# Kernel optimization log

Measured on AMD Instinct MI355X. Metric: run time of the kernel, lower is better.

## Reference

```python
import jax, jax.numpy as jnp
import numpy as np

T, N, E = 4, 20000, 320000
F_IN, EH, NH, GH, OUT = 12, 32, 64, 64, 1
NUM_LAYERS = 2
EB_IN = (EH + 2 * NH) * 2 + GH  # 384
NB_IN = 2 * NH + 2 * EH + GH    # 256
GB_IN = NH + EH + GH            # 160


def setup_inputs() -> dict:
    key = jax.random.key(0)
    ks = jax.random.split(key, 24)
    f32 = jnp.float32
    def w(k, fan_in, shape):
        return jax.random.normal(k, shape, f32) * (1.0 / np.sqrt(fan_in))
    return {
        "node_attr": jax.random.normal(ks[0], (T, N, F_IN), f32),
        "edge_attr": jax.random.normal(ks[1], (T, E, 1), f32),
        "edge_index": jax.random.randint(ks[2], (2, E), 0, N, jnp.int32),
        "sp_L_vals": jax.random.normal(ks[3], (E,), f32),
        "global_attr": jax.random.normal(ks[4], (1, GH), f32),
        "coeff": jnp.full((1,), 0.1, f32),
        "W_ee": w(ks[5], 1, (1, EH)), "b_ee": jnp.zeros((EH,), f32),
        "W_ne": w(ks[6], F_IN, (F_IN, NH)), "b_ne": jnp.zeros((NH,), f32),
        "W_eb": w(ks[7], EB_IN, (EB_IN, EH)), "b_eb": jnp.zeros((EH,), f32),
        "W_nb": w(ks[8], NB_IN, (NB_IN, NH)), "b_nb": jnp.zeros((NH,), f32),
        "W_gb": w(ks[9], GB_IN, (GB_IN, GH)), "b_gb": jnp.zeros((GH,), f32),
        "W_nd1": w(ks[10], NH, (NH, NH)), "b_nd1": jnp.zeros((NH,), f32),
        "W_nd2": w(ks[11], NH, (NH, OUT)), "b_nd2": jnp.zeros((OUT,), f32),
    }


def _forward(node_attr, edge_attr, edge_index, sp_L_vals, global_attr, coeff,
             W_ee, b_ee, W_ne, b_ne, W_eb, b_eb, W_nb, b_nb, W_gb, b_gb,
             W_nd1, b_nd1, W_nd2, b_nd2):
    relu = jax.nn.relu
    s, r = edge_index[0], edge_index[1]
    seg = lambda v, idx: jax.ops.segment_sum(v, idx, num_segments=N)
    c = coeff[0]

    # encoders
    x_enc = relu(node_attr @ W_ne + b_ne)   # [T,N,NH]
    e_enc = relu(edge_attr @ W_ee + b_ee)   # [T,E,EH]

    def run_gn(xT, eT, g0):
        # recurrent GN core over processing steps; hidden (h_x,h_e,h_g) starts at zeros
        def step(carry, inp):
            h_x, h_e, h_g = carry
            x_in, e_in = inp
            gE = jnp.broadcast_to(h_g, (E, GH))
            # EdgeBlock: [edge_in, edge_h, sender_in, sender_h, recv_in, recv_h, global]
            edge_cat = jnp.concatenate(
                [e_in, h_e, x_in[s], h_x[s], x_in[r], h_x[r], gE], axis=-1)
            e_new = relu(edge_cat @ W_eb + b_eb)              # [E,EH]
            sent = seg(e_new, s)                              # scatter_add by sender
            recv = seg(e_new, r)                              # scatter_add by receiver
            gN = jnp.broadcast_to(h_g, (N, GH))
            node_cat = jnp.concatenate([x_in, h_x, sent, recv, gN], axis=-1)
            x_new = relu(node_cat @ W_nb + b_nb)              # [N,NH]
            # GlobalBlock: scatter_mean == plain mean (single graph)
            g_cat = jnp.concatenate(
                [x_new.mean(0, keepdims=True), e_new.mean(0, keepdims=True), h_g], axis=-1)
            g_new = relu(g_cat @ W_gb + b_gb)                 # [1,GH]
            # physics terms (pde='diff'): time derivative = state update,
            # spatial derivative = coeff * (graph-Laplacian action via sp_L edge weights)
            t_der = x_new - h_x
            s_der = c * seg(sp_L_vals[:, None] * (x_new[s] - x_new[r]), r)
            return (x_new, e_new, g_new), (x_new, e_new, g_new, t_der, s_der)
        carry0 = (jnp.zeros((N, NH), jnp.float32), jnp.zeros((E, EH), jnp.float32), g0)
        _, ys = jax.lax.scan(step, carry0, (xT, eT))
        return ys  # xs[T,N,NH], es[T,E,EH], gs[T,1,GH], td[T,N,NH], sd[T,N,NH]

    xs, es, gs, td, sd = run_gn(x_enc, e_enc, global_attr)
    x_pre = x_enc
    for _ in range(NUM_LAYERS - 1):
        x_res = xs + x_pre          # residual node state feeds next GN layer
        x_pre = x_res
        xs, es, gs, td, sd = run_gn(x_res, es, gs[0])

    x_final = xs + x_pre            # add_residual=True final residual
    h = relu(x_final @ W_nd1 + b_nd1)
    out_nodes = h @ W_nd2 + b_nd2   # [T,N,OUT]
    return out_nodes, td, sd


def reference(node_attr, edge_attr, edge_index, sp_L_vals, global_attr, coeff,
              W_ee, b_ee, W_ne, b_ne, W_eb, b_eb, W_nb, b_nb, W_gb, b_gb,
              W_nd1, b_nd1, W_nd2, b_nd2):
    return _forward(node_attr, edge_attr, edge_index, sp_L_vals, global_attr, coeff,
                    W_ee, b_ee, W_ne, b_ne, W_eb, b_eb, W_nb, b_nb, W_gb, b_gb,
                    W_nd1, b_nd1, W_nd2, b_nd2)
```

## Files before the change

kernel.cpp:

```cpp
#include <hip/hip_runtime.h>


typedef __attribute__((ext_vector_type(8))) short s16x8;
typedef __attribute__((ext_vector_type(4))) float f32x4;

#define T_STEPS 4
#define NN 20000
#define NP 20224
#define NE 320000

__device__ __forceinline__ float bf2f(unsigned short h){
  return __uint_as_float(((unsigned)h)<<16);
}
__device__ __forceinline__ unsigned short f2bf(float f){
  unsigned u = __float_as_uint(f);
  return (unsigned short)((u + 0x7fffu + ((u>>16)&1u)) >> 16);
}
__device__ __forceinline__ float loadIn(const void* p, size_t i, int bf){
  return bf ? bf2f(((const unsigned short*)p)[i]) : ((const float*)p)[i];
}
__device__ __forceinline__ void storeOut(void* o, size_t i, float v, int bf){
  if(bf) ((unsigned short*)o)[i] = f2bf(v);
  else   ((float*)o)[i] = v;
}
__device__ __forceinline__ void load8(const float* __restrict__ p, float* v){
  const float4* q4 = (const float4*)p;
  float4 a = q4[0], b = q4[1];
  v[0]=a.x; v[1]=a.y; v[2]=a.z; v[3]=a.w;
  v[4]=b.x; v[5]=b.y; v[6]=b.z; v[7]=b.w;
}
__device__ __forceinline__ int4 pack8(const float* v){
  unsigned p0 = (unsigned)f2bf(v[0]) | ((unsigned)f2bf(v[1])<<16);
  unsigned p1 = (unsigned)f2bf(v[2]) | ((unsigned)f2bf(v[3])<<16);
  unsigned p2 = (unsigned)f2bf(v[4]) | ((unsigned)f2bf(v[5])<<16);
  unsigned p3 = (unsigned)f2bf(v[6]) | ((unsigned)f2bf(v[7])<<16);
  return make_int4((int)p0,(int)p1,(int)p2,(int)p3);
}
__device__ __forceinline__ void unp8(int4 w, float* a){
  unsigned x;
  x=(unsigned)w.x; a[0]=__uint_as_float(x<<16); a[1]=__uint_as_float(x&0xffff0000u);
  x=(unsigned)w.y; a[2]=__uint_as_float(x<<16); a[3]=__uint_as_float(x&0xffff0000u);
  x=(unsigned)w.z; a[4]=__uint_as_float(x<<16); a[5]=__uint_as_float(x&0xffff0000u);
  x=(unsigned)w.w; a[6]=__uint_as_float(x<<16); a[7]=__uint_as_float(x&0xffff0000u);
}

union I4S8 { int4 i; s16x8 s; };

__global__ void probe_kernel(const void* coeff_in, int* flagp, float* coeff_f){
  unsigned short u = ((const unsigned short*)coeff_in)[0];
  float as_bf = bf2f(u);
  int f = (fabsf(as_bf - 0.1f) < 0.02f) ? 1 : 0;
  *flagp = f;
  *coeff_f = f ? as_bf : ((const float*)coeff_in)[0];
}

struct ConvJob { const void* src; float* dst; int n; };
struct ConvJobs { ConvJob j[16]; int cnt; };

__global__ void conv_kernel(ConvJobs jobs, const int* flagp, float* z, int zn){
  int bf = *flagp;
  int tid = blockIdx.x*blockDim.x + threadIdx.x;
  int stride = gridDim.x*blockDim.x;
  for(int q=0;q<jobs.cnt;q++){
    const void* s = jobs.j[q].src; float* d = jobs.j[q].dst; int n = jobs.j[q].n;
    for(int i=tid;i<n;i+=stride) d[i] = loadIn(s, i, bf);
  }
  for(int i=tid;i<zn;i+=stride) z[i]=0.f;
}

__global__ void csr_hist(const int* __restrict__ ei, int* deg_s, int* deg_r,
                         unsigned short* __restrict__ rank_s,
                         unsigned short* __restrict__ rank_r){
  int e = blockIdx.x*256+threadIdx.x;
  rank_s[e] = (unsigned short)atomicAdd(&deg_s[ei[e]],1);
  rank_r[e] = (unsigned short)atomicAdd(&deg_r[ei[NE+e]],1);
}

__global__ void csr_scan(const int* __restrict__ deg_s, int* __restrict__ off_s,
                         const int* __restrict__ deg_r, int* __restrict__ off_r){
  const int CH = NP/256;
  const int* deg = blockIdx.x ? deg_r : deg_s;
  int* off = blockIdx.x ? off_r : off_s;
  int t = threadIdx.x;
  int base = t*CH;
  int s = 0;
  #pragma unroll 8
  for(int i=0;i<CH;i++) s += deg[base+i];
  int lane = t & 63, w = t >> 6;
  int x = s;
  #pragma unroll
  for(int o=1;o<64;o<<=1){
    int y = __shfl_up(x, o, 64);
    if(lane >= o) x += y;
  }
  __shared__ int wtot[4];
  if(lane==63) wtot[w] = x;
  __syncthreads();
  int wbase = 0;
  #pragma unroll
  for(int k=0;k<3;k++) if(k<w) wbase += wtot[k];
  int acc = wbase + x - s;
  #pragma unroll 8
  for(int i=0;i<CH;i++){
    off[base+i]=acc; acc+=deg[base+i];
  }
  if(t==255) off[NN]=acc;
}

__global__ void csr_fill(const int* __restrict__ ei,
                         const int* __restrict__ s_off, const int* __restrict__ r_off,
                         const unsigned short* __restrict__ rank_s,
                         const unsigned short* __restrict__ rank_r,
                         int* __restrict__ csr_s, int* __restrict__ csr_r,
                         int2* __restrict__ sr2){
  int e = blockIdx.x*256+threadIdx.x;
  int s = ei[e], r = ei[NE+e];
  sr2[e] = make_int2(s,r);
  csr_s[s_off[s]+rank_s[e]] = e;
  csr_r[r_off[r]+rank_r[e]] = e;
}

__global__ void pack_w_kernel(const void* __restrict__ W,
                              unsigned short* __restrict__ P, int KW, int NT,
                              const int* flagp){
  int bf = *flagp;
  int idx = blockIdx.x*blockDim.x + threadIdx.x;
  int total = NT*KW*512;
  if(idx>=total) return;
  int j = idx & 7;
  int lane = (idx>>3) & 63;
  int rest = idx >> 9;
  int kw = rest % KW;
  int nt = rest / KW;
  int k = kw*32 + (lane>>4)*8 + j;
  int n = nt*16 + (lane&15);
  P[idx] = f2bf(loadIn(W, (size_t)k*(NT*16) + n, bf));
}

__global__ void node_enc_kernel(const void* __restrict__ na,
                                const float* __restrict__ W, const float* __restrict__ b,
                                unsigned short* __restrict__ xA, const int* flagp){
  __shared__ float arow[4][12];
  int bf = *flagp;
  int lane = threadIdx.x & 63, nl = threadIdx.x >> 6;
  int row = blockIdx.x*4 + nl;
  if(lane<12) arow[nl][lane] = loadIn(na, (size_t)row*12+lane, bf);
  __syncthreads();
  float acc = b[lane];
  #pragma unroll
  for(int k=0;k<12;k++) acc += arow[nl][k]*W[k*64+lane];
  xA[(size_t)row*64+lane] = f2bf(fmaxf(acc,0.f));
}

__global__ __launch_bounds__(256) void edge_block_mfma(
  const int2* __restrict__ sr2,
  const unsigned short* __restrict__ x_in,
  const unsigned short* __restrict__ h_x,
  const void* __restrict__ e_attr,
  int e_attr_off,
  const unsigned short* __restrict__ e_in,
  const unsigned short* __restrict__ h_e,
  const float* __restrict__ g,
  const float* __restrict__ W_ee, const float* __restrict__ b_ee,
  const unsigned short* __restrict__ Wp,
  const float* __restrict__ b_eb,
  unsigned short* __restrict__ e_out,
  float* __restrict__ partial_e,
  const int* flagp)
{
  const int tid = threadIdx.x;
  const int lane = tid&63;
  const int q = lane>>4, m16 = lane&15;
  const int pair = blockIdx.x*4 + (tid>>6);
  const int e0 = pair*32;
  const int eg0 = e0 + m16, eg1 = e0 + 16 + m16;
  const int2 sr0 = sr2[eg0], sr1 = sr2[eg1];
  const int o8 = q*8;
  const int4 z4 = make_int4(0,0,0,0);

  I4S8 A0[12], A1[12];
  if(e_attr){
    int bf = *flagp;
    float a0v = loadIn(e_attr, (size_t)e_attr_off + eg0, bf);
    float a1v = loadIn(e_attr, (size_t)e_attr_off + eg1, bf);
    float v[8];
    #pragma unroll
    for(int j=0;j<8;j++) v[j] = fmaxf(a0v*W_ee[o8+j]+b_ee[o8+j], 0.f);
    A0[0].i = pack8(v);
    #pragma unroll
    for(int j=0;j<8;j++) v[j] = fmaxf(a1v*W_ee[o8+j]+b_ee[o8+j], 0.f);
    A1[0].i = pack8(v);
  } else {
    A0[0].i = ((const int4*)(e_in + (size_t)eg0*32))[q];
    A1[0].i = ((const int4*)(e_in + (size_t)eg1*32))[q];
  }
  A0[1].i = h_e ? ((const int4*)(h_e + (size_t)eg0*32))[q] : z4;
  A1[1].i = h_e ? ((const int4*)(h_e + (size_t)eg1*32))[q] : z4;
  { const int4* p0 = (const int4*)(x_in + (size_t)sr0.x*64);
    const int4* p1 = (const int4*)(x_in + (size_t)sr1.x*64);
    A0[2].i = p0[q]; A1[2].i = p1[q];
    A0[3].i = p0[4+q]; A1[3].i = p1[4+q]; }
  if(h_x){
    const int4* p0 = (const int4*)(h_x + (size_t)sr0.x*64);
    const int4* p1 = (const int4*)(h_x + (size_t)sr1.x*64);
    A0[4].i = p0[q]; A1[4].i = p1[q];
    A0[5].i = p0[4+q]; A1[5].i = p1[4+q];
  } else { A0[4].i=z4; A1[4].i=z4; A0[5].i=z4; A1[5].i=z4; }
  { const int4* p0 = (const int4*)(x_in + (size_t)sr0.y*64);
    const int4* p1 = (const int4*)(x_in + (size_t)sr1.y*64);
    A0[6].i = p0[q]; A1[6].i = p1[q];
    A0[7].i = p0[4+q]; A1[7].i = p1[4+q]; }
  if(h_x){
    const int4* p0 = (const int4*)(h_x + (size_t)sr0.y*64);
    const int4* p1 = (const int4*)(h_x + (size_t)sr1.y*64);
    A0[8].i = p0[q]; A1[8].i = p1[q];
    A0[9].i = p0[4+q]; A1[9].i = p1[4+q];
  } else { A0[8].i=z4; A1[8].i=z4; A0[9].i=z4; A1[9].i=z4; }
  { float v[8];
    load8(g + o8, v);      A0[10].i = pack8(v); A1[10].i = A0[10].i;
    load8(g + 32 + o8, v); A0[11].i = pack8(v); A1[11].i = A0[11].i; }

  f32x4 a00={0.f,0.f,0.f,0.f}, a01={0.f,0.f,0.f,0.f};
  f32x4 a10={0.f,0.f,0.f,0.f}, a11={0.f,0.f,0.f,0.f};
  #pragma unroll
  for(int kw=0;kw<12;kw++){
    s16x8 b0 = *(const s16x8*)(Wp + (size_t)(kw*64 + lane)*8);
    s16x8 b1 = *(const s16x8*)(Wp + (size_t)((12+kw)*64 + lane)*8);
    a00 = __builtin_amdgcn_mfma_f32_16x16x32_bf16(A0[kw].s, b0, a00, 0,0,0);
    a01 = __builtin_amdgcn_mfma_f32_16x16x32_bf16(A0[kw].s, b1, a01, 0,0,0);
    a10 = __builtin_amdgcn_mfma_f32_16x16x32_bf16(A1[kw].s, b0, a10, 0,0,0);
    a11 = __builtin_amdgcn_mfma_f32_16x16x32_bf16(A1[kw].s, b1, a11, 0,0,0);
  }

  float pe0=0.f, pe1=0.f;
  const float bb0 = b_eb[m16], bb1 = b_eb[16+m16];
  #pragma unroll
  for(int r=0;r<4;r++){
    int eg0m = e0 + q*4 + r;
    int eg1m = eg0m + 16;
    float v00 = fmaxf(a00[r]+bb0, 0.f);
    float v01 = fmaxf(a01[r]+bb1, 0.f);
    float v10 = fmaxf(a10[r]+bb0, 0.f);
    float v11 = fmaxf(a11[r]+bb1, 0.f);
    e_out[(size_t)eg0m*32+m16]    = f2bf(v00);
    e_out[(size_t)eg0m*32+16+m16] = f2bf(v01);
    e_out[(size_t)eg1m*32+m16]    = f2bf(v10);
    e_out[(size_t)eg1m*32+16+m16] = f2bf(v11);
    pe0 += v00+v10; pe1 += v01+v11;
  }
  pe0 += __shfl_xor(pe0,16,64); pe0 += __shfl_xor(pe0,32,64);
  pe1 += __shfl_xor(pe1,16,64); pe1 += __shfl_xor(pe1,32,64);
  if(q==0){
    int slot = blockIdx.x & 63;
    atomicAdd(&partial_e[slot*32+m16],    pe0);
    atomicAdd(&partial_e[slot*32+16+m16], pe1);
  }
}

__global__ void aggregate_kernel(const unsigned short* __restrict__ e_new,
  const int* __restrict__ s_off, const int* __restrict__ csr_s,
  const int* __restrict__ r_off, const int* __restrict__ csr_r,
  unsigned short* __restrict__ sentB, unsigned short* __restrict__ recvB)
{
  int node = blockIdx.x*4 + (threadIdx.x>>6);
  int lane = threadIdx.x & 63;
  int f = lane & 31, j = lane >> 5;
  float aS0=0.f, aS1=0.f, aR0=0.f, aR1=0.f;
  {
    int beg = s_off[node], end = s_off[node+1];
    int i = beg + j;
    for(; i+2<end; i+=4){
      aS0 += bf2f(e_new[(size_t)csr_s[i]*32 + f]);
      aS1 += bf2f(e_new[(size_t)csr_s[i+2]*32 + f]);
    }
    for(; i<end; i+=2)
      aS0 += bf2f(e_new[(size_t)csr_s[i]*32 + f]);
  }
  {
    int beg = r_off[node], end = r_off[node+1];
    int i = beg + j;
    for(; i+2<end; i+=4){
      aR0 += bf2f(e_new[(size_t)csr_r[i]*32 + f]);
      aR1 += bf2f(e_new[(size_t)csr_r[i+2]*32 + f]);
    }
    for(; i<end; i+=2)
      aR0 += bf2f(e_new[(size_t)csr_r[i]*32 + f]);
  }
  float accS = aS0+aS1, accR = aR0+aR1;
  accS += __shfl_xor(accS,32,64);
  accR += __shfl_xor(accR,32,64);
  if(j==0){
    sentB[(size_t)node*32+f] = f2bf(accS);
    recvB[(size_t)node*32+f] = f2bf(accR);
  }
}

__global__ __launch_bounds__(256) void node_block_mfma(
  const unsigned short* __restrict__ x_in, const unsigned short* __restrict__ h_x,
  const unsigned short* __restrict__ sentB, const unsigned short* __restrict__ recvB,
  const float* __restrict__ g,
  const unsigned short* __restrict__ Wp,
  const float* __restrict__ b_nb,
  unsigned short* __restrict__ x_out, float* __restrict__ partial_x,
  void* __restrict__ out_base, size_t td_off, int has_td,
  const int* flagp)
{
  const int tid = threadIdx.x, lane = tid&63;
  const int q = lane>>4, m16 = lane&15;
  const int tile = blockIdx.x*4 + (tid>>6);
  if(tile >= NN/16) return;
  const int n0 = tile*16;
  const int ng = n0+m16;
  const int o8 = q*8;
  const int4 z4 = make_int4(0,0,0,0);

  I4S8 A[8];
  { const int4* xp = (const int4*)(x_in + (size_t)ng*64);
    A[0].i = xp[q]; A[1].i = xp[4+q]; }
  if(h_x){ const int4* hp = (const int4*)(h_x + (size_t)ng*64);
    A[2].i = hp[q]; A[3].i = hp[4+q];
  } else { A[2].i = z4; A[3].i = z4; }
  A[4].i = ((const int4*)(sentB + (size_t)ng*32))[q];
  A[5].i = ((const int4*)(recvB + (size_t)ng*32))[q];
  { float v[8];
    load8(g + o8, v);      A[6].i = pack8(v);
    load8(g + 32 + o8, v); A[7].i = pack8(v); }

  f32x4 acc[4];
  #pragma unroll
  for(int nt=0;nt<4;nt++) acc[nt] = (f32x4){0.f,0.f,0.f,0.f};
  #pragma unroll
  for(int kw=0;kw<8;kw++){
    #pragma unroll
    for(int nt=0;nt<4;nt++){
      s16x8 b = *(const s16x8*)(Wp + (size_t)((nt*8+kw)*64 + lane)*8);
      acc[nt] = __builtin_amdgcn_mfma_f32_16x16x32_bf16(A[kw].s, b, acc[nt], 0,0,0);
    }
  }

  int bf = has_td ? *flagp : 0;
  float ps[4] = {0.f,0.f,0.f,0.f};
  #pragma unroll
  for(int r=0;r<4;r++){
    int nodeg = n0 + q*4 + r;
    #pragma unroll
    for(int nt=0;nt<4;nt++){
      int col = nt*16 + m16;
      float vv = fmaxf(acc[nt][r] + b_nb[col], 0.f);
      x_out[(size_t)nodeg*64+col] = f2bf(vv);
      if(has_td){
        float hxv = h_x ? bf2f(h_x[(size_t)nodeg*64+col]) : 0.f;
        storeOut(out_base, td_off + (size_t)nodeg*64+col, vv - hxv, bf);
      }
      ps[nt] += vv;
    }
  }
  #pragma unroll
  for(int nt=0;nt<4;nt++){
    ps[nt] += __shfl_xor(ps[nt],16,64);
    ps[nt] += __shfl_xor(ps[nt],32,64);
  }
  if(q==0){
    int slot = blockIdx.x & 63;
    #pragma unroll
    for(int nt=0;nt<4;nt++)
      atomicAdd(&partial_x[slot*64 + nt*16 + m16], ps[nt]);
  }
}

__global__ void global_block_kernel(float* __restrict__ partial_x,
  float* __restrict__ partial_e, const float* __restrict__ h_g,
  const float* __restrict__ W_gb, const float* __restrict__ b_gb,
  float* __restrict__ g_out)
{
  __shared__ float gcat[160];
  __shared__ float red[4][64];
  int tid = threadIdx.x;
  if(tid<64){
    float sx = 0.f;
    #pragma unroll 8
    for(int i=0;i<64;i++) sx += partial_x[i*64+tid];
    gcat[tid] = sx * (1.0f/(float)NN);
  } else if(tid<96){
    int j = tid-64;
    float se = 0.f;
    #pragma unroll 8
    for(int i=0;i<64;i++) se += partial_e[i*32+j];
    gcat[64+j] = se * (1.0f/(float)NE);
  } else if(tid<160){
    gcat[tid] = h_g[tid-96];
  }
  __syncthreads();
  int j = tid&63, c = tid>>6;
  float acc = 0.f;
  #pragma unroll 8
  for(int k=c*40;k<c*40+40;k++) acc += gcat[k]*W_gb[k*64+j];
  red[c][j] = acc;
  __syncthreads();
  for(int i=tid;i<2048;i+=256) partial_e[i]=0.f;
  for(int i=tid;i<4096;i+=256) partial_x[i]=0.f;
  if(tid<64){
    float a = red[0][tid]+red[1][tid]+red[2][tid]+red[3][tid] + b_gb[tid];
    g_out[tid] = fmaxf(a, 0.f);
  }
}

__global__ void sder_csr_kernel(const int2* __restrict__ sr2,
  const void* __restrict__ spL, const unsigned short* __restrict__ x_new,
  const int* __restrict__ r_off, const int* __restrict__ csr_r,
  const float* __restrict__ coeff, void* __restrict__ out_base, size_t off,
  const int* flagp)
{
  int bf = *flagp;
  int lane = threadIdx.x&63, nl = threadIdx.x>>6;
  int node = blockIdx.x*4+nl;
  float xn = bf2f(x_new[(size_t)node*64+lane]);
  float a0=0.f, a1=0.f, a2=0.f, a3=0.f;
  int beg = r_off[node], end = r_off[node+1];
  int i = beg;
  for(; i+4<=end; i+=4){
    int e1 = csr_r[i], e2 = csr_r[i+1], e3 = csr_r[i+2], e4 = csr_r[i+3];
    float w1 = loadIn(spL, e1, bf), w2 = loadIn(spL, e2, bf);
    float w3 = loadIn(spL, e3, bf), w4 = loadIn(spL, e4, bf);
    int s1 = sr2[e1].x, s2 = sr2[e2].x, s3 = sr2[e3].x, s4 = sr2[e4].x;
    a0 += w1*(bf2f(x_new[(size_t)s1*64+lane])-xn);
    a1 += w2*(bf2f(x_new[(size_t)s2*64+lane])-xn);
    a2 += w3*(bf2f(x_new[(size_t)s3*64+lane])-xn);
    a3 += w4*(bf2f(x_new[(size_t)s4*64+lane])-xn);
  }
  for(; i<end; i++){
    int e1 = csr_r[i];
    float w1 = loadIn(spL, e1, bf);
    a0 += w1*(bf2f(x_new[(size_t)sr2[e1].x*64+lane])-xn);
  }
  storeOut(out_base, off + (size_t)node*64+lane, coeff[0]*((a0+a1)+(a2+a3)), bf);
}

__global__ void add_bf16_kernel(const unsigned short* __restrict__ a,
  const unsigned short* __restrict__ b, unsigned short* __restrict__ c, int n){
  int i = blockIdx.x*blockDim.x+threadIdx.x;
  int stride = gridDim.x*blockDim.x;
  for(;i<n;i+=stride) c[i] = f2bf(bf2f(a[i])+bf2f(b[i]));
}

__global__ __launch_bounds__(256) void decoder_kernel(
  const unsigned short* __restrict__ xs, const unsigned short* __restrict__ xr,
  const unsigned short* __restrict__ WpD,
  const float* __restrict__ b1, const float* __restrict__ W2,
  const float* __restrict__ b2,
  void* __restrict__ out_base, const int* flagp)
{
  const int tid=threadIdx.x, lane=tid&63;
  const int q=lane>>4, m16=lane&15;
  const int tile = blockIdx.x*4 + (tid>>6);
  const int row0 = tile*16;
  const int rg = row0 + m16;

  I4S8 A[2];
  #pragma unroll
  for(int kw=0;kw<2;kw++){
    int4 xa = ((const int4*)(xs + (size_t)rg*64 + kw*32))[q];
    int4 xb = ((const int4*)(xr + (size_t)rg*64 + kw*32))[q];
    float va[8], vb[8], v[8];
    unp8(xa, va); unp8(xb, vb);
    #pragma unroll
    for(int j=0;j<8;j++) v[j] = va[j]+vb[j];
    A[kw].i = pack8(v);
  }

  f32x4 acc[4];
  #pragma unroll
  for(int nt=0;nt<4;nt++) acc[nt] = (f32x4){0.f,0.f,0.f,0.f};
  #pragma unroll
  for(int kw=0;kw<2;kw++){
    #pragma unroll
    for(int nt=0;nt<4;nt++){
      s16x8 b = *(const s16x8*)(WpD + (size_t)((nt*2+kw)*64 + lane)*8);
      acc[nt] = __builtin_amdgcn_mfma_f32_16x16x32_bf16(A[kw].s, b, acc[nt], 0,0,0);
    }
  }

  float val[4];
  #pragma unroll
  for(int r=0;r<4;r++){
    float s = 0.f;
    #pragma unroll
    for(int nt=0;nt<4;nt++){
      int col = nt*16 + m16;
      s += fmaxf(acc[nt][r] + b1[col], 0.f) * W2[col];
    }
    val[r] = s;
  }
  #pragma unroll
  for(int o=1;o<16;o<<=1){
    #pragma unroll
    for(int r=0;r<4;r++) val[r] += __shfl_xor(val[r], o, 64);
  }
  if(m16==0){
    int bf = *flagp;
    float bb = b2[0];
    #pragma unroll
    for(int r=0;r<4;r++)
      storeOut(out_base, (size_t)(row0 + q*4 + r), val[r] + bb, bf);
  }
}

extern "C" void kernel_launch(void* const* d_in, const int* in_sizes, int n_in,
                              void* d_out, int out_size, void* d_ws, size_t ws_size,
                              hipStream_t stream){
  const void* node_attr = d_in[0];
  const void* edge_attr = d_in[1];
  const int*  ei        = (const int*)d_in[2];
  const void* spL       = d_in[3];
  const void* gattr     = d_in[4];
  const void* coeff_in  = d_in[5];
  const void* W_ee_in = d_in[6];  const void* b_ee_in = d_in[7];
  const void* W_ne_in = d_in[8];  const void* b_ne_in = d_in[9];
  const void* W_eb_in = d_in[10]; const void* b_eb_in = d_in[11];
  const void* W_nb_in = d_in[12]; const void* b_nb_in = d_in[13];
  const void* W_gb_in = d_in[14]; const void* b_gb_in = d_in[15];
  const void* W_nd1_in= d_in[16]; const void* b_nd1_in= d_in[17];
  const void* W_nd2_in= d_in[18]; const void* b_nd2_in= d_in[19];

  float* ws = (float*)d_ws;
  float* W_ee_f = ws;             float* b_ee_f = W_ee_f+32;
  float* W_ne_f = b_ee_f+32;      float* b_ne_f = W_ne_f+768;
  float* W_gb_f = b_ne_f+64;      float* b_gb_f = W_gb_f+10240;
  float* W_nd1_f= b_gb_f+64;      float* b_nd1_f= W_nd1_f+4096;
  float* W_nd2_f= b_nd1_f+64;     float* b_nd2_f= W_nd2_f+64;
  float* b_eb_f = b_nd2_f+1;      float* b_nb_f = b_eb_f+32;
  float* coeff_f= b_nb_f+64;
  int*   flagp  = (int*)(ws + 15523);
  float* gbuf   = ws + 15524;
  float* part_e = ws + 16100;
  float* part_x = part_e + 2048;
  int*   deg_s  = (int*)(part_x + 4096);
  int*   deg_r  = deg_s + NP;
  int*   s_off  = deg_r + NP;
  int*   r_off  = s_off + NP+1;
  unsigned short* rank_s = (unsigned short*)(r_off + NP+1);
  unsigned short* rank_r = rank_s + NE;
  int*   csr_s  = (int*)(rank_r + NE);
  int*   csr_r  = csr_s + NE;
  size_t iend   = (size_t)((int*)(csr_r + NE) - (int*)ws);
  iend = (iend + 3) & ~(size_t)3;
  int2*  sr2    = (int2*)(ws + iend);
  unsigned short* sentB = (unsigned short*)(sr2 + NE);
  unsigned short* recvB = sentB + (size_t)NN*32;
  unsigned short* eBuf  = recvB + (size_t)NN*32;
  unsigned short* xA    = eBuf + (size_t)T_STEPS*NE*32;
  unsigned short* xB    = xA + (size_t)T_STEPS*NN*64;
  unsigned short* xC    = xB + (size_t)T_STEPS*NN*64;
  unsigned short* WpE   = xC + (size_t)T_STEPS*NN*64;
  unsigned short* WpN   = WpE + 12288;
  unsigned short* WpD   = WpN + 16384;

  probe_kernel<<<1,1,0,stream>>>(coeff_in, flagp, coeff_f);

  ConvJobs jobs; int c=0;
  auto add=[&](const void* s, float* d, int n){ jobs.j[c].src=s; jobs.j[c].dst=d; jobs.j[c].n=n; c++; };
  add(W_ee_in,W_ee_f,32);   add(b_ee_in,b_ee_f,32);
  add(W_ne_in,W_ne_f,768);  add(b_ne_in,b_ne_f,64);
  add(W_gb_in,W_gb_f,10240);add(b_gb_in,b_gb_f,64);
  add(W_nd1_in,W_nd1_f,4096);add(b_nd1_in,b_nd1_f,64);
  add(W_nd2_in,W_nd2_f,64); add(b_nd2_in,b_nd2_f,1);
  add(b_eb_in,b_eb_f,32);   add(b_nb_in,b_nb_f,64);
  add(gattr,gbuf,64);
  jobs.cnt=c;
  conv_kernel<<<64,256,0,stream>>>(jobs, flagp, part_e, 2048+4096+2*NP);

  csr_hist<<<NE/256,256,0,stream>>>(ei, deg_s, deg_r, rank_s, rank_r);
  csr_scan<<<2,256,0,stream>>>(deg_s, s_off, deg_r, r_off);
  csr_fill<<<NE/256,256,0,stream>>>(ei, s_off, r_off, rank_s, rank_r, csr_s, csr_r, sr2);

  pack_w_kernel<<<48,256,0,stream>>>(W_eb_in, WpE, 12, 2, flagp);
  pack_w_kernel<<<64,256,0,stream>>>(W_nb_in, WpN, 8, 4, flagp);
  pack_w_kernel<<<16,256,0,stream>>>(W_nd1_in, WpD, 2, 4, flagp);

  node_enc_kernel<<<T_STEPS*NN/4,256,0,stream>>>(node_attr, W_ne_f, b_ne_f, xA, flagp);

  const size_t td_base = (size_t)T_STEPS*NN;
  const size_t sd_base = td_base + (size_t)T_STEPS*NN*64;

  for(int layer=0; layer<2; layer++){
    for(int t=0;t<T_STEPS;t++){
      const unsigned short* x_in = (layer==0? xA : xC) + (size_t)t*NN*64;
      const unsigned short* h_x  = (t>0)? xB + (size_t)(t-1)*NN*64 : nullptr;
      const unsigned short* h_e  = (t>0)? eBuf + (size_t)(t-1)*NE*32 : nullptr;
      const float* gptr = (layer==0)? gbuf + t*64
                                    : (t==0? gbuf+1*64 : gbuf+(4+t)*64);
      float*       gout = (layer==0)? gbuf+(1+t)*64 : gbuf+(5+t)*64;
      const void*  eat  = (layer==0)? edge_attr : nullptr;
      const unsigned short* e_in = (layer==0)? nullptr : eBuf + (size_t)t*NE*32;
      unsigned short*       e_out= eBuf + (size_t)t*NE*32;

      edge_block_mfma<<<NE/128,256,0,stream>>>(sr2, x_in, h_x, eat, t*NE, e_in, h_e, gptr,
          W_ee_f, b_ee_f, WpE, b_eb_f, e_out, part_e, flagp);

      aggregate_kernel<<<NN/4,256,0,stream>>>(e_out, s_off, csr_s, r_off, csr_r,
          sentB, recvB);

      unsigned short* x_out = xB + (size_t)t*NN*64;
      size_t td_off = td_base + (size_t)t*NN*64;
      node_block_mfma<<<(NN/16+3)/4,256,0,stream>>>(x_in, h_x, sentB, recvB, gptr,
          WpN, b_nb_f, x_out, part_x, d_out, td_off, (layer==1)?1:0, flagp);

      global_block_kernel<<<1,256,0,stream>>>(part_x, part_e, gptr, W_gb_f, b_gb_f, gout);

      if(layer==1){
        sder_csr_kernel<<<NN/4,256,0,stream>>>(sr2, spL, x_out, r_off, csr_r,
            coeff_f, d_out, sd_base + (size_t)t*NN*64, flagp);
      }
    }
    if(layer==0){
      add_bf16_kernel<<<2048,256,0,stream>>>(xA, xB, xC, T_STEPS*NN*64);
    }
  }

  decoder_kernel<<<(T_STEPS*NN/16+3)/4,256,0,stream>>>(xB, xC, WpD,
      b_nd1_f, W_nd2_f, b_nd2_f, d_out, flagp);
}
```

Measured before the change: 939.7 us.

## Swap MFMA operands to transpose accumulator layout for vectorized stores; unroll aggregation

Swaps the A and B operands of the MFMA calls in the edge, node and decoder kernels, so each lane holds four consecutive output columns of one row instead of one column across four rows. This allows packed 8-byte bf16 stores and float4 bias loads in place of scattered 2-byte stores, and a single cross-lane reduction in the decoder. The cost is more shuffles and atomics for the partial sums in the edge and node kernels. The CSR aggregation loop is also unrolled to four independent accumulators to expose more memory-level parallelism.

```diff
diff --git a/kernel.cpp b/kernel.cpp
--- a/kernel.cpp
+++ b/kernel.cpp
@@ -35,6 +35,16 @@
   unsigned p2 = (unsigned)f2bf(v[4]) | ((unsigned)f2bf(v[5])<<16);
   unsigned p3 = (unsigned)f2bf(v[6]) | ((unsigned)f2bf(v[7])<<16);
   return make_int4((int)p0,(int)p1,(int)p2,(int)p3);
+}
+__device__ __forceinline__ int2 pack4(const float* v){
+  unsigned u0 = (unsigned)f2bf(v[0]) | ((unsigned)f2bf(v[1])<<16);
+  unsigned u1 = (unsigned)f2bf(v[2]) | ((unsigned)f2bf(v[3])<<16);
+  return make_int2((int)u0,(int)u1);
+}
+__device__ __forceinline__ void unp4(int2 w, float* a){
+  unsigned x;
+  x=(unsigned)w.x; a[0]=__uint_as_float(x<<16); a[1]=__uint_as_float(x&0xffff0000u);
+  x=(unsigned)w.y; a[2]=__uint_as_float(x<<16); a[3]=__uint_as_float(x&0xffff0000u);
 }
 __device__ __forceinline__ void unp8(int4 w, float* a){
   unsigned x;
@@ -226,34 +236,45 @@
   for(int kw=0;kw<12;kw++){
     s16x8 b0 = *(const s16x8*)(Wp + (size_t)(kw*64 + lane)*8);
     s16x8 b1 = *(const s16x8*)(Wp + (size_t)((12+kw)*64 + lane)*8);
-    a00 = __builtin_amdgcn_mfma_f32_16x16x32_bf16(A0[kw].s, b0, a00, 0,0,0);
-    a01 = __builtin_amdgcn_mfma_f32_16x16x32_bf16(A0[kw].s, b1, a01, 0,0,0);
-    a10 = __builtin_amdgcn_mfma_f32_16x16x32_bf16(A1[kw].s, b0, a10, 0,0,0);
-    a11 = __builtin_amdgcn_mfma_f32_16x16x32_bf16(A1[kw].s, b1, a11, 0,0,0);
-  }
-
-  float pe0=0.f, pe1=0.f;
-  const float bb0 = b_eb[m16], bb1 = b_eb[16+m16];
+    a00 = __builtin_amdgcn_mfma_f32_16x16x32_bf16(b0, A0[kw].s, a00, 0,0,0);
+    a01 = __builtin_amdgcn_mfma_f32_16x16x32_bf16(b1, A0[kw].s, a01, 0,0,0);
+    a10 = __builtin_amdgcn_mfma_f32_16x16x32_bf16(b0, A1[kw].s, a10, 0,0,0);
+    a11 = __builtin_amdgcn_mfma_f32_16x16x32_bf16(b1, A1[kw].s, a11, 0,0,0);
+  }
+
+  const float4 bb0 = *(const float4*)(b_eb + q*4);
+  const float4 bb1 = *(const float4*)(b_eb + 16 + q*4);
+  float v00[4], v01[4], v10[4], v11[4], p0[4], p1[4];
   #pragma unroll
   for(int r=0;r<4;r++){
-    int eg0m = e0 + q*4 + r;
-    int eg1m = eg0m + 16;
-    float v00 = fmaxf(a00[r]+bb0, 0.f);
-    float v01 = fmaxf(a01[r]+bb1, 0.f);
-    float v10 = fmaxf(a10[r]+bb0, 0.f);
-    float v11 = fmaxf(a11[r]+bb1, 0.f);
-    e_out[(size_t)eg0m*32+m16]    = f2bf(v00);
-    e_out[(size_t)eg0m*32+16+m16] = f2bf(v01);
-    e_out[(size_t)eg1m*32+m16]    = f2bf(v10);
-    e_out[(size_t)eg1m*32+16+m16] = f2bf(v11);
-    pe0 += v00+v10; pe1 += v01+v11;
-  }
-  pe0 += __shfl_xor(pe0,16,64); pe0 += __shfl_xor(pe0,32,64);
-  pe1 += __shfl_xor(pe1,16,64); pe1 += __shfl_xor(pe1,32,64);
-  if(q==0){
+    float b0v = (&bb0.x)[r], b1v = (&bb1.x)[r];
+    v00[r] = fmaxf(a00[r]+b0v, 0.f);
+    v01[r] = fmaxf(a01[r]+b1v, 0.f);
+    v10[r] = fmaxf(a10[r]+b0v, 0.f);
+    v11[r] = fmaxf(a11[r]+b1v, 0.f);
+    p0[r] = v00[r]+v10[r];
+    p1[r] = v01[r]+v11[r];
+  }
+  *(int2*)(e_out + (size_t)eg0*32 + q*4)      = pack4(v00);
+  *(int2*)(e_out + (size_t)eg0*32 + 16 + q*4) = pack4(v01);
+  *(int2*)(e_out + (size_t)eg1*32 + q*4)      = pack4(v10);
+  *(int2*)(e_out + (size_t)eg1*32 + 16 + q*4) = pack4(v11);
+
+  #pragma unroll
+  for(int m=1;m<16;m<<=1){
+    #pragma unroll
+    for(int r=0;r<4;r++){
+      p0[r] += __shfl_xor(p0[r], m, 64);
+      p1[r] += __shfl_xor(p1[r], m, 64);
+    }
+  }
+  if(m16==0){
     int slot = blockIdx.x & 63;
-    atomicAdd(&partial_e[slot*32+m16],    pe0);
-    atomicAdd(&partial_e[slot*32+16+m16], pe1);
+    #pragma unroll
+    for(int r=0;r<4;r++){
+      atomicAdd(&partial_e[slot*32 + q*4+r],      p0[r]);
+      atomicAdd(&partial_e[slot*32 + 16 + q*4+r], p1[r]);
+    }
   }
 }
 
@@ -265,28 +286,33 @@
   int node = blockIdx.x*4 + (threadIdx.x>>6);
   int lane = threadIdx.x & 63;
   int f = lane & 31, j = lane >> 5;
-  float aS0=0.f, aS1=0.f, aR0=0.f, aR1=0.f;
+  float aS0=0.f, aS1=0.f, aS2=0.f, aS3=0.f;
+  float aR0=0.f, aR1=0.f, aR2=0.f, aR3=0.f;
   {
-    int beg = s_off[node], end = s_off[node+1];
-    int i = beg + j;
-    for(; i+2<end; i+=4){
+    int end = s_off[node+1];
+    int i = s_off[node] + j;
+    for(; i+6<end; i+=8){
       aS0 += bf2f(e_new[(size_t)csr_s[i]*32 + f]);
       aS1 += bf2f(e_new[(size_t)csr_s[i+2]*32 + f]);
+      aS2 += bf2f(e_new[(size_t)csr_s[i+4]*32 + f]);
+      aS3 += bf2f(e_new[(size_t)csr_s[i+6]*32 + f]);
     }
     for(; i<end; i+=2)
       aS0 += bf2f(e_new[(size_t)csr_s[i]*32 + f]);
   }
   {
-    int beg = r_off[node], end = r_off[node+1];
-    int i = beg + j;
-    for(; i+2<end; i+=4){
+    int end = r_off[node+1];
+    int i = r_off[node] + j;
+    for(; i+6<end; i+=8){
       aR0 += bf2f(e_new[(size_t)csr_r[i]*32 + f]);
       aR1 += bf2f(e_new[(size_t)csr_r[i+2]*32 + f]);
+      aR2 += bf2f(e_new[(size_t)csr_r[i+4]*32 + f]);
+      aR3 += bf2f(e_new[(size_t)csr_r[i+6]*32 + f]);
     }
     for(; i<end; i+=2)
       aR0 += bf2f(e_new[(size_t)csr_r[i]*32 + f]);
   }
-  float accS = aS0+aS1, accR = aR0+aR1;
+  float accS = (aS0+aS1)+(aS2+aS3), accR = (aR0+aR1)+(aR2+aR3);
   accS += __shfl_xor(accS,32,64);
   accR += __shfl_xor(accR,32,64);
   if(j==0){
@@ -334,37 +360,47 @@
     #pragma unroll
     for(int nt=0;nt<4;nt++){
       s16x8 b = *(const s16x8*)(Wp + (size_t)((nt*8+kw)*64 + lane)*8);
-      acc[nt] = __builtin_amdgcn_mfma_f32_16x16x32_bf16(A[kw].s, b, acc[nt], 0,0,0);
+      acc[nt] = __builtin_amdgcn_mfma_f32_16x16x32_bf16(b, A[kw].s, acc[nt], 0,0,0);
     }
   }
 
   int bf = has_td ? *flagp : 0;
-  float ps[4] = {0.f,0.f,0.f,0.f};
-  #pragma unroll
-  for(int r=0;r<4;r++){
-    int nodeg = n0 + q*4 + r;
-    #pragma unroll
-    for(int nt=0;nt<4;nt++){
-      int col = nt*16 + m16;
-      float vv = fmaxf(acc[nt][r] + b_nb[col], 0.f);
-      x_out[(size_t)nodeg*64+col] = f2bf(vv);
-      if(has_td){
-        float hxv = h_x ? bf2f(h_x[(size_t)nodeg*64+col]) : 0.f;
-        storeOut(out_base, td_off + (size_t)nodeg*64+col, vv - hxv, bf);
-      }
-      ps[nt] += vv;
-    }
-  }
+  float ps[4][4];
   #pragma unroll
   for(int nt=0;nt<4;nt++){
-    ps[nt] += __shfl_xor(ps[nt],16,64);
-    ps[nt] += __shfl_xor(ps[nt],32,64);
-  }
-  if(q==0){
+    const float4 bb = *(const float4*)(b_nb + nt*16 + q*4);
+    float v[4];
+    #pragma unroll
+    for(int r=0;r<4;r++) v[r] = fmaxf(acc[nt][r] + (&bb.x)[r], 0.f);
+    *(int2*)(x_out + (size_t)ng*64 + nt*16 + q*4) = pack4(v);
+    if(has_td){
+      float hx[4] = {0.f,0.f,0.f,0.f};
+      if(h_x) unp4(*(const int2*)(h_x + (size_t)ng*64 + nt*16 + q*4), hx);
+      float td[4];
+      #pragma unroll
+      for(int r=0;r<4;r++) td[r] = v[r]-hx[r];
+      size_t idx = td_off + (size_t)ng*64 + nt*16 + q*4;
+      if(bf) *(int2*)((unsigned short*)out_base + idx) = pack4(td);
+      else   *(float4*)((float*)out_base + idx) = make_float4(td[0],td[1],td[2],td[3]);
+    }
+    #pragma unroll
+    for(int r=0;r<4;r++) ps[nt][r] = v[r];
+  }
+  #pragma unroll
+  for(int m=1;m<16;m<<=1){
+    #pragma unroll
+    for(int nt=0;nt<4;nt++)
+      #pragma unroll
+      for(int r=0;r<4;r++)
+        ps[nt][r] += __shfl_xor(ps[nt][r], m, 64);
+  }
+  if(m16==0){
     int slot = blockIdx.x & 63;
     #pragma unroll
     for(int nt=0;nt<4;nt++)
-      atomicAdd(&partial_x[slot*64 + nt*16 + m16], ps[nt]);
+      #pragma unroll
+      for(int r=0;r<4;r++)
+        atomicAdd(&partial_x[slot*64 + nt*16 + q*4 + r], ps[nt][r]);
   }
 }
 
@@ -476,32 +512,23 @@
     #pragma unroll
     for(int nt=0;nt<4;nt++){
       s16x8 b = *(const s16x8*)(WpD + (size_t)((nt*2+kw)*64 + lane)*8);
-      acc[nt] = __builtin_amdgcn_mfma_f32_16x16x32_bf16(A[kw].s, b, acc[nt], 0,0,0);
-    }
-  }
-
-  float val[4];
-  #pragma unroll
-  for(int r=0;r<4;r++){
-    float s = 0.f;
-    #pragma unroll
-    for(int nt=0;nt<4;nt++){
-      int col = nt*16 + m16;
-      s += fmaxf(acc[nt][r] + b1[col], 0.f) * W2[col];
-    }
-    val[r] = s;
-  }
-  #pragma unroll
-  for(int o=1;o<16;o<<=1){
-    #pragma unroll
-    for(int r=0;r<4;r++) val[r] += __shfl_xor(val[r], o, 64);
-  }
-  if(m16==0){
-    int bf = *flagp;
-    float bb = b2[0];
+      acc[nt] = __builtin_amdgcn_mfma_f32_16x16x32_bf16(b, A[kw].s, acc[nt], 0,0,0);
+    }
+  }
+
+  float val = 0.f;
+  #pragma unroll
+  for(int nt=0;nt<4;nt++){
+    const float4 bb = *(const float4*)(b1 + nt*16 + q*4);
+    const float4 w2 = *(const float4*)(W2 + nt*16 + q*4);
     #pragma unroll
     for(int r=0;r<4;r++)
-      storeOut(out_base, (size_t)(row0 + q*4 + r), val[r] + bb, bf);
+      val += fmaxf(acc[nt][r] + (&bb.x)[r], 0.f) * (&w2.x)[r];
+  }
+  val += __shfl_xor(val, 16, 64);
+  val += __shfl_xor(val, 32, 64);
+  if(q==0){
+    storeOut(out_base, (size_t)rg, val + b2[0], *flagp);
   }
 }
 
```

Result: slower. 1.046 ms (+11.3%).
